# Performance work log

Measured on AMD Instinct MI355X. Metric: run time of the kernel, lower is better.

The kernel has to match this reference:

```python
import jax, jax.numpy as jnp
import numpy as np

BS, NQ, NC, NT = 32, 300, 2001, 25


def setup_inputs() -> dict:
    key = jax.random.key(0)
    k1, k2 = jax.random.split(key)
    pred_logits = jax.random.normal(k1, (BS, NQ, NC), dtype=jnp.float32)
    targets = jax.random.randint(k2, (BS, NT), 0, 2000, dtype=jnp.int32)
    return {"pred_logits": pred_logits, "targets": targets}


def _lsa(C):
    """Jonker-Volgenant shortest-augmenting-path LSAP (same algorithm as
    scipy.optimize.linear_sum_assignment). C: [r, c] with r <= c, minimize.
    Returns col4row: for each row, the assigned column."""
    r, c = C.shape
    u = np.zeros(r, np.float64)
    v = np.zeros(c, np.float64)
    col4row = np.full(r, -1, np.intp)
    row4col = np.full(c, -1, np.intp)
    for cur in range(r):
        shortest = np.full(c, np.inf)
        path = np.full(c, -1, np.intp)
        SC = np.zeros(c, bool)
        sr_rows = []
        minVal = 0.0
        i = cur
        sink = -1
        while sink == -1:
            sr_rows.append(i)
            rem = np.where(~SC)[0]  # columns not yet scanned
            d = minVal + C[i, rem] - u[i] - v[rem]
            upd = d < shortest[rem]
            shortest[rem[upd]] = d[upd]
            path[rem[upd]] = i
            jpos = rem[np.argmin(shortest[rem])]
            minVal = shortest[jpos]
            SC[jpos] = True
            if row4col[jpos] == -1:
                sink = jpos
            else:
                i = row4col[jpos]
        # dual updates (keep alternating-tree edges tight)
        u[cur] += minVal
        for irow in sr_rows:
            if irow != cur:
                u[irow] += minVal - shortest[col4row[irow]]
        scj = np.where(SC)[0]
        v[scj] -= minVal - shortest[scj]
        # augment along the found path
        j = sink
        while True:
            i = path[j]
            row4col[j] = i
            col4row[i], j = j, col4row[i]
            if i == cur:
                break
    return col4row


def _match(cost_np):
    """cost_np: [nq, nt] with nq >= nt. Same result as scipy's
    linear_sum_assignment: (row_ind sorted ascending, col_ind)."""
    col4row = _lsa(cost_np.T)  # per target -> matched query index
    order = np.argsort(col4row, kind="stable")
    return col4row[order], order


def reference(pred_logits, targets):
    bs, nq, _ = pred_logits.shape
    nt = targets.shape[1]
    # softmax over classes, then gather the target-class probabilities
    prob = jax.nn.softmax(pred_logits, axis=-1)            # [bs, nq, nc]
    idx = jnp.broadcast_to(targets[:, None, :], (bs, nq, nt))
    cost = -jnp.take_along_axis(prob, idx, axis=2)          # [bs, nq, nt]
    # host-side Hungarian assignment per batch element (as in the original,
    # which calls scipy.linear_sum_assignment on CPU per element)
    cost_np = np.asarray(jax.device_get(cost), dtype=np.float64)
    rows, cols = [], []
    for b in range(bs):
        ri, ci = _match(cost_np[b])
        rows.append(ri)
        cols.append(ci)
    row_inds = jnp.asarray(np.stack(rows), dtype=jnp.int64 if jax.config.jax_enable_x64 else jnp.int32)
    col_inds = jnp.asarray(np.stack(cols), dtype=jnp.int64 if jax.config.jax_enable_x64 else jnp.int32)
    return (row_inds, col_inds)
```

## Files before the change

kernel.cpp:

```cpp
#include <hip/hip_runtime.h>
#include <math.h>
#include <float.h>

#define BS 32
#define NQ 300
#define NC 2001
#define NT 25
#define KSLOT 5

__global__ __launch_bounds__(64) void cost_kernel(const float* __restrict__ logits,
                                                  const int* __restrict__ targets,
                                                  float* __restrict__ costT) {
    int row = blockIdx.x;
    int b = row / NQ;
    int q = row - b * NQ;
    const float* lp = logits + (size_t)row * NC;
    int lane = threadIdx.x;

    int head = (4 - (row & 3)) & 3;
    int nvec = (NC - head) >> 2;
    int tail = (NC - head) & 3;
    const float4* vp = (const float4*)(lp + head);

    float m = -FLT_MAX;
    for (int k = lane; k < nvec; k += 64) {
        float4 x = vp[k];
        m = fmaxf(m, fmaxf(fmaxf(x.x, x.y), fmaxf(x.z, x.w)));
    }
    if (lane < head) m = fmaxf(m, lp[lane]);
    if (lane < tail) m = fmaxf(m, lp[head + 4 * nvec + lane]);
    for (int off = 1; off < 64; off <<= 1) m = fmaxf(m, __shfl_xor(m, off));

    float s = 0.f;
    for (int k = lane; k < nvec; k += 64) {
        float4 x = vp[k];
        s += expf(x.x - m) + expf(x.y - m) + expf(x.z - m) + expf(x.w - m);
    }
    if (lane < head) s += expf(lp[lane] - m);
    if (lane < tail) s += expf(lp[head + 4 * nvec + lane] - m);
    for (int off = 1; off < 64; off <<= 1) s += __shfl_xor(s, off);

    if (lane < NT) {
        int t = targets[b * NT + lane];
        float p = expf(lp[t] - m) / s;
        costT[((size_t)b * NT + lane) * NQ + q] = -p;
    }
}

__global__ __launch_bounds__(64) void lsap_kernel(const float* __restrict__ costT,
                                                  int* __restrict__ out) {
    int b = blockIdx.x;
    int tid = threadIdx.x;

    __shared__ float   C[NT * NQ];
    __shared__ double  u[NT];
    __shared__ double  shortestS[NQ];
    __shared__ int     pathS[NQ];
    __shared__ int     row4col[NQ];
    __shared__ int     col4row[NT];
    __shared__ int     sr_rows[NT];

    {
        const float4* src4 = (const float4*)(costT + (size_t)b * NT * NQ);
        float4* dst4 = (float4*)C;
        for (int k = tid; k < (NT * NQ) / 4; k += 64) dst4[k] = src4[k];
    }
    for (int j = tid; j < NQ; j += 64) row4col[j] = -1;
    if (tid < NT) { u[tid] = 0.0; col4row[tid] = -1; }

    double v_r[KSLOT];
    bool   own[KSLOT];
    #pragma unroll
    for (int k = 0; k < KSLOT; ++k) { v_r[k] = 0.0; own[k] = (tid + 64 * k) < NQ; }
    __syncthreads();

    for (int cur = 0; cur < NT; ++cur) {
        double shortest_r[KSLOT];
        int    path_r[KSLOT];
        bool   sc_r[KSLOT];
        #pragma unroll
        for (int k = 0; k < KSLOT; ++k) { shortest_r[k] = INFINITY; path_r[k] = -1; sc_r[k] = false; }

        double minVal = 0.0;
        int i = cur;
        int nsr = 0;
        int sink = -1;

        while (sink == -1) {
            if (tid == 0) sr_rows[nsr] = i;
            nsr++;
            double ui = u[i];

            double lmin = INFINITY;
            #pragma unroll
            for (int k = 0; k < KSLOT; ++k) {
                if (own[k] && !sc_r[k]) {
                    int j = tid + 64 * k;
                    double d = ((minVal + (double)C[i * NQ + j]) - ui) - v_r[k];
                    if (d < shortest_r[k]) { shortest_r[k] = d; path_r[k] = i; }
                    if (shortest_r[k] < lmin) lmin = shortest_r[k];
                }
            }
            double gmin = lmin;
            #pragma unroll
            for (int off = 1; off < 64; off <<= 1) {
                double o = __shfl_xor(gmin, off);
                if (o < gmin) gmin = o;
            }
            int jpos = -1;
            #pragma unroll
            for (int k = 0; k < KSLOT; ++k) {
                unsigned long long mk =
                    __ballot(own[k] && !sc_r[k] && shortest_r[k] == gmin);
                if (jpos < 0 && mk) jpos = 64 * k + __builtin_ctzll(mk);
            }
            minVal = gmin;

            int kj = jpos >> 6, lj = jpos & 63;
            if (tid == lj) {
                sc_r[kj] = true;
                pathS[jpos] = path_r[kj];
            }
            if (tid == 0) shortestS[jpos] = gmin;

            int r = row4col[jpos];
            if (r == -1) sink = jpos; else i = r;
            __syncthreads();
        }

        if (tid == 0) {
            u[cur] += minVal;
        } else if (tid < nsr) {
            int irow = sr_rows[tid];
            u[irow] += minVal - shortestS[col4row[irow]];
        }
        #pragma unroll
        for (int k = 0; k < KSLOT; ++k) {
            if (sc_r[k]) v_r[k] -= minVal - shortest_r[k];
        }
        __syncthreads();

        if (tid == 0) {
            int j = sink;
            while (true) {
                int ii = pathS[j];
                row4col[j] = ii;
                int nj = col4row[ii];
                col4row[ii] = j;
                j = nj;
                if (ii == cur) break;
            }
        }
        __syncthreads();
    }

    if (tid < NT) {
        int myq = col4row[tid];
        int rank = 0;
        for (int k = 0; k < NT; ++k) {
            if (col4row[k] < myq) rank++;
        }
        out[b * NT + rank]           = myq;
        out[BS * NT + b * NT + rank] = tid;
    }
}

extern "C" void kernel_launch(void* const* d_in, const int* in_sizes, int n_in,
                              void* d_out, int out_size, void* d_ws, size_t ws_size,
                              hipStream_t stream) {
    const float* logits  = (const float*)d_in[0];
    const int*   targets = (const int*)d_in[1];
    int*         out     = (int*)d_out;
    float*       costT   = (float*)d_ws;

    cost_kernel<<<BS * NQ, 64, 0, stream>>>(logits, targets, costT);
    lsap_kernel<<<BS, 64, 0, stream>>>(costT, out);
}
```

Measured before the change: 164.8 us.

## Add greedy row-min warm start to LSAP and register-cache logits in softmax

Before the shortest-augmenting-path loop, the LSAP kernel now initializes row duals u to each row's minimum cost and greedily assigns each row to a free column achieving that minimum. Rows already assigned are skipped, which cuts the number of serial augmentation phases. The cost kernel also holds each lane's logits in registers so the second softmax pass does not reload them from global memory. The warm start changes the dual state the algorithm begins from, so tie-breaking and the final assignment could in principle differ from the scipy-equivalent reference.

```diff
diff --git a/kernel.cpp b/kernel.cpp
--- a/kernel.cpp
+++ b/kernel.cpp
@@ -22,22 +22,26 @@
     int tail = (NC - head) & 3;
     const float4* vp = (const float4*)(lp + head);
 
-    float m = -FLT_MAX;
-    for (int k = lane; k < nvec; k += 64) {
-        float4 x = vp[k];
+    float4 xr[8];
+    int cnt = 0;
+    for (int k = lane; k < nvec; k += 64) xr[cnt++] = vp[k];
+    float hv = (lane < head) ? lp[lane] : -FLT_MAX;
+    float tv = (lane < tail) ? lp[head + 4 * nvec + lane] : -FLT_MAX;
+
+    float m = fmaxf(hv, tv);
+    for (int t = 0; t < cnt; ++t) {
+        float4 x = xr[t];
         m = fmaxf(m, fmaxf(fmaxf(x.x, x.y), fmaxf(x.z, x.w)));
     }
-    if (lane < head) m = fmaxf(m, lp[lane]);
-    if (lane < tail) m = fmaxf(m, lp[head + 4 * nvec + lane]);
     for (int off = 1; off < 64; off <<= 1) m = fmaxf(m, __shfl_xor(m, off));
 
     float s = 0.f;
-    for (int k = lane; k < nvec; k += 64) {
-        float4 x = vp[k];
+    for (int t = 0; t < cnt; ++t) {
+        float4 x = xr[t];
         s += expf(x.x - m) + expf(x.y - m) + expf(x.z - m) + expf(x.w - m);
     }
-    if (lane < head) s += expf(lp[lane] - m);
-    if (lane < tail) s += expf(lp[head + 4 * nvec + lane] - m);
+    if (lane < head) s += expf(hv - m);
+    if (lane < tail) s += expf(tv - m);
     for (int off = 1; off < 64; off <<= 1) s += __shfl_xor(s, off);
 
     if (lane < NT) {
@@ -66,15 +70,52 @@
         for (int k = tid; k < (NT * NQ) / 4; k += 64) dst4[k] = src4[k];
     }
     for (int j = tid; j < NQ; j += 64) row4col[j] = -1;
-    if (tid < NT) { u[tid] = 0.0; col4row[tid] = -1; }
+    if (tid < NT) col4row[tid] = -1;
 
     double v_r[KSLOT];
     bool   own[KSLOT];
+    bool   free_r[KSLOT];
     #pragma unroll
-    for (int k = 0; k < KSLOT; ++k) { v_r[k] = 0.0; own[k] = (tid + 64 * k) < NQ; }
+    for (int k = 0; k < KSLOT; ++k) {
+        v_r[k] = 0.0;
+        own[k] = (tid + 64 * k) < NQ;
+        free_r[k] = own[k];
+    }
     __syncthreads();
 
+    if (tid < NT) {
+        int base = tid * NQ;
+        float m0 = FLT_MAX, m1 = FLT_MAX, m2 = FLT_MAX, m3 = FLT_MAX;
+        for (int j = 0; j < NQ; j += 4) {
+            m0 = fminf(m0, C[base + j]);
+            m1 = fminf(m1, C[base + j + 1]);
+            m2 = fminf(m2, C[base + j + 2]);
+            m3 = fminf(m3, C[base + j + 3]);
+        }
+        u[tid] = (double)fminf(fminf(m0, m1), fminf(m2, m3));
+    }
+    __syncthreads();
+
+    for (int i = 0; i < NT; ++i) {
+        float rm = (float)u[i];
+        int jm = -1;
+        #pragma unroll
+        for (int k = 0; k < KSLOT; ++k) {
+            int j = tid + 64 * k;
+            int jc = (j < NQ) ? j : (NQ - 1);
+            unsigned long long mk = __ballot(free_r[k] && (C[i * NQ + jc] == rm));
+            if (jm < 0 && mk) jm = 64 * k + __builtin_ctzll(mk);
+        }
+        if (jm >= 0) {
+            if (tid == (jm & 63)) free_r[jm >> 6] = false;
+            if (tid == 0) { row4col[jm] = i; col4row[i] = jm; }
+        }
+    }
+    __syncthreads();
+
     for (int cur = 0; cur < NT; ++cur) {
+        if (col4row[cur] != -1) continue;
+
         double shortest_r[KSLOT];
         int    path_r[KSLOT];
         bool   sc_r[KSLOT];
```

Measured after the change: 199.2 us. 20.9% more time.
